# Kernel optimization log

Hardware: AMD Instinct MI355X
Metric: run time of the kernel (lower is better)

The kernel has to match this reference:

```python
import jax, jax.numpy as jnp
import numpy as np

N, D, M, H, FF, L = 8192, 14, 36, 256, 2048, 2  # rows, d_model, material feats, mlp hidden, ffn, layers
EPS = 1e-5


def _ln(x, g, b):
    mu = jnp.mean(x, axis=-1, keepdims=True)
    var = jnp.mean((x - mu) ** 2, axis=-1, keepdims=True)
    return (x - mu) * jax.lax.rsqrt(var + EPS) * g + b


def setup_inputs() -> dict:
    key = jax.random.key(0)
    ks = iter(jax.random.split(key, 32))
    p = lambda shape, fan: jax.random.normal(next(ks), shape, jnp.float32) * (fan ** -0.5)
    return {
        "x": jax.random.normal(next(ks), (N, D), jnp.float32),
        "y": jax.random.normal(next(ks), (N, M), jnp.float32),
        # 2 post-LN TransformerEncoderLayers (nhead=1, dim_feedforward=2048, relu)
        "attn_wqkv": p((L, 3 * D, D), D), "attn_bqkv": p((L, 3 * D), D),
        "attn_wo": p((L, D, D), D), "attn_bo": p((L, D), D),
        "ln1_g": jnp.ones((L, D)), "ln1_b": jnp.zeros((L, D)),
        "ff_w1": p((L, FF, D), D), "ff_b1": p((L, FF), D),
        "ff_w2": p((L, D, FF), FF), "ff_b2": p((L, D), FF),
        "ln2_g": jnp.ones((L, D)), "ln2_b": jnp.zeros((L, D)),
        "fc1_w": p((D, D), D), "fc1_b": p((D,), D),
        "fc2_w": p((1, D), D), "fc2_b": p((1,), D),
        "fc3_w": p((H, D + M + 1), D + M + 1), "fc3_b": p((H,), D + M + 1),
        "fc4_w": p((H, H), H), "fc4_b": p((H,), H),
        "fc5_w": p((1, H), H), "fc5_b": p((1,), H),
    }


def reference(x, y, attn_wqkv, attn_bqkv, attn_wo, attn_bo, ln1_g, ln1_b,
              ff_w1, ff_b1, ff_w2, ff_b2, ln2_g, ln2_b,
              fc1_w, fc1_b, fc2_w, fc2_b, fc3_w, fc3_b, fc4_w, fc4_b, fc5_w, fc5_b):
    h = x  # [N, D]; batch of size 1 squeezed away
    for l in range(L):
        qkv = h @ attn_wqkv[l].T + attn_bqkv[l]            # [N, 3D]
        q, k, v = jnp.split(qkv, 3, axis=-1)
        scores = (q @ k.T) * (D ** -0.5)                   # [N, N]
        a = jax.nn.softmax(scores, axis=-1) @ v            # [N, D]
        a = a @ attn_wo[l].T + attn_bo[l]
        h = _ln(h + a, ln1_g[l], ln1_b[l])
        f = jax.nn.relu(h @ ff_w1[l].T + ff_b1[l]) @ ff_w2[l].T + ff_b2[l]
        h = _ln(h + f, ln2_g[l], ln2_b[l])
    x1 = h @ fc1_w.T + fc1_b                               # [N, D]
    size_out = (x1 @ fc2_w.T + fc2_b)[:, 0]                # [N]

    # batched replacement of the per-row python loop
    size_int = size_out.astype(jnp.int32)                  # trunc toward zero, like .int()
    size_f = size_int.astype(jnp.float32)[:, None]         # [N, 1]
    reg_in = jnp.concatenate([size_f, x, y], axis=1)       # [N, 1+D+M]
    r = jax.nn.relu(reg_in @ fc3_w.T + fc3_b)
    r = jax.nn.relu(r @ fc4_w.T + fc4_b)
    reg_values = (r @ fc5_w.T + fc5_b)[:, 0]               # [N]
    reg_values = jnp.where(size_int != 0, reg_values, 0.0)
    return size_out, reg_values
```

## Files before the change

### kernel.cpp

```cpp
#include <hip/hip_runtime.h>
#include <math.h>

#define NN 8192
#define DD 14
#define DP 16
#define FF 2048
#define HID 256
#define LN_EPS 1e-5f
#define NCH 16
#define NFCH 8
#define QSCALE (1.4426950408889634f / 3.7416573867739413f)

typedef short bf16x8 __attribute__((ext_vector_type(8)));
typedef float f32x4 __attribute__((ext_vector_type(4)));

#define LOAD16(dst, srcp) { \
  const float4* _p = (const float4*)(srcp); \
  float4 _a = _p[0], _b = _p[1], _c = _p[2], _d = _p[3]; \
  dst[0]=_a.x; dst[1]=_a.y; dst[2]=_a.z; dst[3]=_a.w; \
  dst[4]=_b.x; dst[5]=_b.y; dst[6]=_b.z; dst[7]=_b.w; \
  dst[8]=_c.x; dst[9]=_c.y; dst[10]=_c.z; dst[11]=_c.w; \
  dst[12]=_d.x; dst[13]=_d.y; dst[14]=_d.z; dst[15]=_d.w; }

#define STORE16(dstp, src) { \
  float4* _p = (float4*)(dstp); \
  _p[0] = make_float4(src[0], src[1], src[2], src[3]); \
  _p[1] = make_float4(src[4], src[5], src[6], src[7]); \
  _p[2] = make_float4(src[8], src[9], src[10], src[11]); \
  _p[3] = make_float4(src[12], src[13], src[14], src[15]); }

static __device__ __forceinline__ float fast_exp2(float x) {
#if __has_builtin(__builtin_amdgcn_exp2f)
  return __builtin_amdgcn_exp2f(x);
#else
  return exp2f(x);
#endif
}

static __device__ __forceinline__ unsigned short bf_hi(float x) {
  return (unsigned short)(__float_as_uint(x) >> 16);
}
static __device__ __forceinline__ float bf_hi_f(float x) {
  return __uint_as_float(__float_as_uint(x) & 0xffff0000u);
}

static __device__ __forceinline__ void split8(const float* pv, bf16x8* ph, bf16x8* pl) {
  #pragma unroll
  for (int i = 0; i < 8; i++) {
    unsigned int u = __float_as_uint(pv[i]);
    (*ph)[i] = (short)(u >> 16);
    float rr = pv[i] - __uint_as_float(u & 0xffff0000u);
    (*pl)[i] = (short)(__float_as_uint(rr) >> 16);
  }
}

static __device__ __forceinline__ void qkv_compute_store(
    int r, const float* hr, const float* __restrict__ wqkv,
    const float* __restrict__ bqkv, unsigned int* __restrict__ Qpack,
    unsigned int* __restrict__ KB1, unsigned int* __restrict__ KB2,
    unsigned short* __restrict__ VhiT, unsigned short* __restrict__ VloT) {
  float q[14], k[14], v[14];
  #pragma unroll 6
  for (int c = 0; c < 42; c++) {
    const float* w = wqkv + c * 14;
    float s = bqkv[c];
    #pragma unroll
    for (int d = 0; d < 14; d++) s = fmaf(hr[d], w[d], s);
    if (c < 14)       q[c] = s * QSCALE;
    else if (c < 28)  k[c - 14] = s;
    else              v[c - 28] = s;
  }
  unsigned int qp[16], k1[16], k2[16];
  unsigned short qh[14], ql[14], kh[14], kl[14];
  #pragma unroll
  for (int d = 0; d < 14; d++) {
    qh[d] = bf_hi(q[d]);
    ql[d] = bf_hi(q[d] - bf_hi_f(q[d]));
    kh[d] = bf_hi(k[d]);
    kl[d] = bf_hi(k[d] - bf_hi_f(k[d]));
  }
  #pragma unroll
  for (int i = 0; i < 7; i++) {
    qp[i]     = (unsigned int)qh[2*i] | ((unsigned int)qh[2*i+1] << 16);
    qp[8 + i] = (unsigned int)ql[2*i] | ((unsigned int)ql[2*i+1] << 16);
    k1[i]     = (unsigned int)kh[2*i] | ((unsigned int)kh[2*i+1] << 16);
    k1[8 + i] = k1[i];
    k2[i]     = (unsigned int)kl[2*i] | ((unsigned int)kl[2*i+1] << 16);
    k2[8 + i] = k2[i];
  }
  qp[7] = 0; qp[15] = 0; k1[7] = 0; k1[15] = 0; k2[7] = 0; k2[15] = 0;
  uint4* Qp4 = (uint4*)(Qpack + (size_t)r * 16);
  uint4* K14 = (uint4*)(KB1 + (size_t)r * 16);
  uint4* K24 = (uint4*)(KB2 + (size_t)r * 16);
  #pragma unroll
  for (int i = 0; i < 4; i++) {
    Qp4[i] = make_uint4(qp[4*i], qp[4*i+1], qp[4*i+2], qp[4*i+3]);
    K14[i] = make_uint4(k1[4*i], k1[4*i+1], k1[4*i+2], k1[4*i+3]);
    K24[i] = make_uint4(k2[4*i], k2[4*i+1], k2[4*i+2], k2[4*i+3]);
  }
  #pragma unroll
  for (int d = 0; d < 14; d++) {
    VhiT[(size_t)d * NN + r] = bf_hi(v[d]);
    VloT[(size_t)d * NN + r] = bf_hi(v[d] - bf_hi_f(v[d]));
  }
  VhiT[(size_t)14 * NN + r] = 0x3F80;
  VhiT[(size_t)15 * NN + r] = 0;
  VloT[(size_t)14 * NN + r] = 0;
  VloT[(size_t)15 * NN + r] = 0;
}

static __device__ __forceinline__ void store_apack(unsigned int* dst, const float* o) {
  unsigned int qp[16];
  unsigned short hh[14], ll[14];
  #pragma unroll
  for (int d = 0; d < 14; d++) {
    hh[d] = bf_hi(o[d]);
    ll[d] = bf_hi(o[d] - bf_hi_f(o[d]));
  }
  #pragma unroll
  for (int i = 0; i < 7; i++) {
    qp[i]     = (unsigned int)hh[2*i] | ((unsigned int)hh[2*i+1] << 16);
    qp[8 + i] = (unsigned int)ll[2*i] | ((unsigned int)ll[2*i+1] << 16);
  }
  qp[7] = 0; qp[15] = 0;
  uint4* d4 = (uint4*)dst;
  #pragma unroll
  for (int i = 0; i < 4; i++)
    d4[i] = make_uint4(qp[4*i], qp[4*i+1], qp[4*i+2], qp[4*i+3]);
}

__global__ void pack_all(const float* __restrict__ w3, const float* __restrict__ w4,
                         const float* __restrict__ ffw1, const float* __restrict__ ffw2,
                         const float* __restrict__ x, const float* __restrict__ wqkv,
                         const float* __restrict__ bqkv, float* __restrict__ h,
                         unsigned int* __restrict__ Qpack,
                         unsigned int* __restrict__ KB1, unsigned int* __restrict__ KB2,
                         unsigned short* __restrict__ VhiT, unsigned short* __restrict__ VloT,
                         unsigned short* __restrict__ B3h, unsigned short* __restrict__ B3l,
                         unsigned short* __restrict__ B4h, unsigned short* __restrict__ B4l,
                         unsigned int* __restrict__ W1B1, unsigned int* __restrict__ W1B2,
                         unsigned short* __restrict__ W2h, unsigned short* __restrict__ W2l) {
  const int blk = blockIdx.x, tid = threadIdx.x;
  if (blk < 32) {
    int t = blk * 256 + tid;
    int lane = t & 63, ks = (t >> 6) & 7, nt = t >> 9;
    int n = nt * 16 + (lane & 15);
    int k0 = ks * 32 + (lane >> 4) * 8;
    unsigned int h4[4], l4[4];
    #pragma unroll
    for (int jj = 0; jj < 4; jj++) {
      unsigned short h2[2], l2[2];
      #pragma unroll
      for (int e = 0; e < 2; e++) {
        float v = w4[(size_t)n * 256 + k0 + jj * 2 + e];
        h2[e] = bf_hi(v);
        l2[e] = bf_hi(v - bf_hi_f(v));
      }
      h4[jj] = (unsigned int)h2[0] | ((unsigned int)h2[1] << 16);
      l4[jj] = (unsigned int)l2[0] | ((unsigned int)l2[1] << 16);
    }
    ((uint4*)B4h)[t] = make_uint4(h4[0], h4[1], h4[2], h4[3]);
    ((uint4*)B4l)[t] = make_uint4(l4[0], l4[1], l4[2], l4[3]);
    if (ks < 2) {
      int fi = (nt * 2 + ks) * 64 + lane;
      #pragma unroll
      for (int jj = 0; jj < 4; jj++) {
        unsigned short h2[2], l2[2];
        #pragma unroll
        for (int e = 0; e < 2; e++) {
          int k = k0 + jj * 2 + e;
          float v = (k < 51) ? w3[(size_t)n * 51 + k] : 0.f;
          h2[e] = bf_hi(v);
          l2[e] = bf_hi(v - bf_hi_f(v));
        }
        h4[jj] = (unsigned int)h2[0] | ((unsigned int)h2[1] << 16);
        l4[jj] = (unsigned int)l2[0] | ((unsigned int)l2[1] << 16);
      }
      ((uint4*)B3h)[fi] = make_uint4(h4[0], h4[1], h4[2], h4[3]);
      ((uint4*)B3l)[fi] = make_uint4(l4[0], l4[1], l4[2], l4[3]);
    }
  } else if (blk < 48) {
    int t = (blk - 32) * 256 + tid;
    int l = t >> 11, j = t & 2047;
    const float* wrow = ffw1 + ((size_t)l * FF + j) * 14;
    unsigned int k1[16], k2[16];
    unsigned short kh[14], kl[14];
    #pragma unroll
    for (int d = 0; d < 14; d++) {
      float v = wrow[d];
      kh[d] = bf_hi(v);
      kl[d] = bf_hi(v - bf_hi_f(v));
    }
    #pragma unroll
    for (int i = 0; i < 7; i++) {
      k1[i] = (unsigned int)kh[2*i] | ((unsigned int)kh[2*i+1] << 16);
      k1[8 + i] = k1[i];
      k2[i] = (unsigned int)kl[2*i] | ((unsigned int)kl[2*i+1] << 16);
      k2[8 + i] = k2[i];
    }
    k1[7] = 0; k1[15] = 0; k2[7] = 0; k2[15] = 0;
    uint4* d1 = (uint4*)(W1B1 + (size_t)t * 16);
    uint4* d2 = (uint4*)(W1B2 + (size_t)t * 16);
    #pragma unroll
    for (int i = 0; i < 4; i++) {
      d1[i] = make_uint4(k1[4*i], k1[4*i+1], k1[4*i+2], k1[4*i+3]);
      d2[i] = make_uint4(k2[4*i], k2[4*i+1], k2[4*i+2], k2[4*i+3]);
    }
  } else if (blk < 64) {
    int t = (blk - 48) * 256 + tid;
    int l = t >> 11, j = t & 2047;
    #pragma unroll
    for (int d = 0; d < 16; d++) {
      float v = (d < 14) ? ffw2[((size_t)l * 14 + d) * FF + j] : 0.f;
      W2h[((size_t)l * 16 + d) * FF + j] = bf_hi(v);
      W2l[((size_t)l * 16 + d) * FF + j] = bf_hi(v - bf_hi_f(v));
    }
  } else {
    int r = (blk - 64) * 256 + tid;
    float hr[16];
    #pragma unroll
    for (int d = 0; d < 14; d++) hr[d] = x[(size_t)r * 14 + d];
    hr[14] = 0.f; hr[15] = 0.f;
    STORE16(h + (size_t)r * DP, hr);
    qkv_compute_store(r, hr, wqkv, bqkv, Qpack, KB1, KB2, VhiT, VloT);
  }
}

__global__ __launch_bounds__(256, 4) void attn_mfma(
    const unsigned int* __restrict__ Qpack, const unsigned int* __restrict__ KB1,
    const unsigned int* __restrict__ KB2, const unsigned short* __restrict__ VhiT,
    const unsigned short* __restrict__ VloT, float* __restrict__ part) {
  __shared__ float Plds[4][32][36];
  const int tid = threadIdx.x;
  const int wave = tid >> 6;
  const int lane = tid & 63;
  const int lo4 = lane & 15;
  const int hi4 = lane >> 4;
  const int qbase = blockIdx.x * 128 + wave * 32;
  const int kbase0 = blockIdx.y * 512;

  const bf16x8* Qp = (const bf16x8*)Qpack;
  const bf16x8* B1 = (const bf16x8*)KB1;
  const bf16x8* B2 = (const bf16x8*)KB2;
  const bf16x8* Vh = (const bf16x8*)VhiT;
  const bf16x8* Vl = (const bf16x8*)VloT;

  bf16x8 aQ0 = Qp[(size_t)(qbase + lo4) * 4 + hi4];
  bf16x8 aQ1 = Qp[(size_t)(qbase + 16 + lo4) * 4 + hi4];
  f32x4 acc0 = {0.f, 0.f, 0.f, 0.f};
  f32x4 acc1 = {0.f, 0.f, 0.f, 0.f};
  const f32x4 zero = {0.f, 0.f, 0.f, 0.f};

  for (int c = 0; c < 16; c++) {
    const int kb = kbase0 + c * 32;
    bf16x8 b1g0 = B1[(size_t)(kb + lo4) * 4 + hi4];
    bf16x8 b2g0 = B2[(size_t)(kb + lo4) * 4 + hi4];
    bf16x8 b1g1 = B1[(size_t)(kb + 16 + lo4) * 4 + hi4];
    bf16x8 b2g1 = B2[(size_t)(kb + 16 + lo4) * 4 + hi4];
    bf16x8 vh = Vh[(size_t)lo4 * 1024 + (kb >> 3) + hi4];
    bf16x8 vl = Vl[(size_t)lo4 * 1024 + (kb >> 3) + hi4];

    f32x4 s00 = __builtin_amdgcn_mfma_f32_16x16x32_bf16(aQ0, b1g0, zero, 0, 0, 0);
    f32x4 s01 = __builtin_amdgcn_mfma_f32_16x16x32_bf16(aQ0, b1g1, zero, 0, 0, 0);
    f32x4 s10 = __builtin_amdgcn_mfma_f32_16x16x32_bf16(aQ1, b1g0, zero, 0, 0, 0);
    f32x4 s11 = __builtin_amdgcn_mfma_f32_16x16x32_bf16(aQ1, b1g1, zero, 0, 0, 0);
    s00 = __builtin_amdgcn_mfma_f32_16x16x32_bf16(aQ0, b2g0, s00, 0, 0, 0);
    s01 = __builtin_amdgcn_mfma_f32_16x16x32_bf16(aQ0, b2g1, s01, 0, 0, 0);
    s10 = __builtin_amdgcn_mfma_f32_16x16x32_bf16(aQ1, b2g0, s10, 0, 0, 0);
    s11 = __builtin_amdgcn_mfma_f32_16x16x32_bf16(aQ1, b2g1, s11, 0, 0, 0);
    #pragma unroll
    for (int reg = 0; reg < 4; reg++) {
      Plds[wave][hi4 * 4 + reg][lo4]           = fast_exp2(s00[reg]);
      Plds[wave][hi4 * 4 + reg][16 + lo4]      = fast_exp2(s01[reg]);
      Plds[wave][16 + hi4 * 4 + reg][lo4]      = fast_exp2(s10[reg]);
      Plds[wave][16 + hi4 * 4 + reg][16 + lo4] = fast_exp2(s11[reg]);
    }
    __asm__ volatile("s_waitcnt lgkmcnt(0)" ::: "memory");
    const float4* p0 = (const float4*)&Plds[wave][lo4][hi4 * 8];
    const float4* p1 = (const float4*)&Plds[wave][16 + lo4][hi4 * 8];
    float4 a0 = p0[0], a1 = p0[1], c0 = p1[0], c1 = p1[1];
    float pv0[8] = {a0.x, a0.y, a0.z, a0.w, a1.x, a1.y, a1.z, a1.w};
    float pv1[8] = {c0.x, c0.y, c0.z, c0.w, c1.x, c1.y, c1.z, c1.w};
    bf16x8 ph0, pl0, ph1, pl1;
    split8(pv0, &ph0, &pl0);
    split8(pv1, &ph1, &pl1);
    acc0 = __builtin_amdgcn_mfma_f32_16x16x32_bf16(ph0, vh, acc0, 0, 0, 0);
    acc1 = __builtin_amdgcn_mfma_f32_16x16x32_bf16(ph1, vh, acc1, 0, 0, 0);
    acc0 = __builtin_amdgcn_mfma_f32_16x16x32_bf16(pl0, vh, acc0, 0, 0, 0);
    acc1 = __builtin_amdgcn_mfma_f32_16x16x32_bf16(pl1, vh, acc1, 0, 0, 0);
    acc0 = __builtin_amdgcn_mfma_f32_16x16x32_bf16(ph0, vl, acc0, 0, 0, 0);
    acc1 = __builtin_amdgcn_mfma_f32_16x16x32_bf16(ph1, vl, acc1, 0, 0, 0);
    __asm__ volatile("s_waitcnt lgkmcnt(0)" ::: "memory");
  }
  float* pbase = part + (size_t)blockIdx.y * NN * 16;
  #pragma unroll
  for (int reg = 0; reg < 4; reg++) {
    int row0 = qbase + hi4 * 4 + reg;
    pbase[(size_t)row0 * 16 + lo4] = acc0[reg];
    pbase[(size_t)(row0 + 16) * 16 + lo4] = acc1[reg];
  }
}

__global__ void attn_comb_ln1(float* __restrict__ h, const float* __restrict__ part,
                              const float* __restrict__ wo, const float* __restrict__ bo,
                              const float* __restrict__ g, const float* __restrict__ b,
                              unsigned int* __restrict__ Hpack) {
  int t = blockIdx.x * 128 + threadIdx.x;
  int r = t >> 2, q = t & 3;
  float L = 0.f;
  float A[14];
  #pragma unroll
  for (int d = 0; d < 14; d++) A[d] = 0.f;
  #pragma unroll
  for (int c = q; c < NCH; c += 4) {
    float p[16];
    LOAD16(p, part + ((size_t)c * NN + r) * 16);
    L += p[14];
    #pragma unroll
    for (int d = 0; d < 14; d++) A[d] += p[d];
  }
  #pragma unroll
  for (int off = 1; off < 4; off <<= 1) {
    L += __shfl_xor(L, off, 64);
    #pragma unroll
    for (int d = 0; d < 14; d++) A[d] += __shfl_xor(A[d], off, 64);
  }
  if (q == 0) {
    float inv = 1.f / L;
    float a[14];
    #pragma unroll
    for (int d = 0; d < 14; d++) a[d] = A[d] * inv;
    float hr[16];
    LOAD16(hr, h + (size_t)r * DP);
    float xx[14];
    #pragma unroll
    for (int i = 0; i < 14; i++) {
      float s = bo[i];
      #pragma unroll
      for (int d = 0; d < 14; d++) s = fmaf(wo[i * 14 + d], a[d], s);
      xx[i] = hr[i] + s;
    }
    float mu = 0.f;
    #pragma unroll
    for (int i = 0; i < 14; i++) mu += xx[i];
    mu *= (1.f / 14.f);
    float var = 0.f;
    #pragma unroll
    for (int i = 0; i < 14; i++) { float tt = xx[i] - mu; var = fmaf(tt, tt, var); }
    var *= (1.f / 14.f);
    float rs = rsqrtf(var + LN_EPS);
    float o[16];
    #pragma unroll
    for (int i = 0; i < 14; i++) o[i] = fmaf((xx[i] - mu) * rs, g[i], b[i]);
    o[14] = 0.f; o[15] = 0.f;
    STORE16(h + (size_t)r * DP, o);
    store_apack(Hpack + (size_t)r * 16, o);
  }
}

__global__ __launch_bounds__(256, 4) void ffn_mfma(
    const unsigned int* __restrict__ Hpack, const unsigned int* __restrict__ W1B1,
    const unsigned int* __restrict__ W1B2, const unsigned short* __restrict__ W2h,
    const unsigned short* __restrict__ W2l, const float* __restrict__ b1,
    float* __restrict__ part) {
  __shared__ float Plds[4][32][36];
  const int tid = threadIdx.x;
  const int wave = tid >> 6;
  const int lane = tid & 63;
  const int lo4 = lane & 15;
  const int hi4 = lane >> 4;
  const int qbase = blockIdx.x * 128 + wave * 32;
  const int jbase0 = blockIdx.y * 256;

  const bf16x8* Hp = (const bf16x8*)Hpack;
  const bf16x8* B1 = (const bf16x8*)W1B1;
  const bf16x8* B2 = (const bf16x8*)W1B2;
  const bf16x8* Vh = (const bf16x8*)W2h;
  const bf16x8* Vl = (const bf16x8*)W2l;

  bf16x8 aH0 = Hp[(size_t)(qbase + lo4) * 4 + hi4];
  bf16x8 aH1 = Hp[(size_t)(qbase + 16 + lo4) * 4 + hi4];
  f32x4 acc0 = {0.f, 0.f, 0.f, 0.f};
  f32x4 acc1 = {0.f, 0.f, 0.f, 0.f};
  const f32x4 zero = {0.f, 0.f, 0.f, 0.f};

  for (int c = 0; c < 8; c++) {
    const int jb = jbase0 + c * 32;
    bf16x8 b1g0 = B1[(size_t)(jb + lo4) * 4 + hi4];
    bf16x8 b2g0 = B2[(size_t)(jb + lo4) * 4 + hi4];
    bf16x8 b1g1 = B1[(size_t)(jb + 16 + lo4) * 4 + hi4];
    bf16x8 b2g1 = B2[(size_t)(jb + 16 + lo4) * 4 + hi4];
    bf16x8 vh = Vh[(size_t)lo4 * 256 + (jb >> 3) + hi4];
    bf16x8 vl = Vl[(size_t)lo4 * 256 + (jb >> 3) + hi4];
    float bb0 = b1[jb + lo4];
    float bb1 = b1[jb + 16 + lo4];

    f32x4 s00 = __builtin_amdgcn_mfma_f32_16x16x32_bf16(aH0, b1g0, zero, 0, 0, 0);
    f32x4 s01 = __builtin_amdgcn_mfma_f32_16x16x32_bf16(aH0, b1g1, zero, 0, 0, 0);
    f32x4 s10 = __builtin_amdgcn_mfma_f32_16x16x32_bf16(aH1, b1g0, zero, 0, 0, 0);
    f32x4 s11 = __builtin_amdgcn_mfma_f32_16x16x32_bf16(aH1, b1g1, zero, 0, 0, 0);
    s00 = __builtin_amdgcn_mfma_f32_16x16x32_bf16(aH0, b2g0, s00, 0, 0, 0);
    s01 = __builtin_amdgcn_mfma_f32_16x16x32_bf16(aH0, b2g1, s01, 0, 0, 0);
    s10 = __builtin_amdgcn_mfma_f32_16x16x32_bf16(aH1, b2g0, s10, 0, 0, 0);
    s11 = __builtin_amdgcn_mfma_f32_16x16x32_bf16(aH1, b2g1, s11, 0, 0, 0);
    #pragma unroll
    for (int reg = 0; reg < 4; reg++) {
      Plds[wave][hi4 * 4 + reg][lo4]           = fmaxf(s00[reg] + bb0, 0.f);
      Plds[wave][hi4 * 4 + reg][16 + lo4]      = fmaxf(s01[reg] + bb1, 0.f);
      Plds[wave][16 + hi4 * 4 + reg][lo4]      = fmaxf(s10[reg] + bb0, 0.f);
      Plds[wave][16 + hi4 * 4 + reg][16 + lo4] = fmaxf(s11[reg] + bb1, 0.f);
    }
    __asm__ volatile("s_waitcnt lgkmcnt(0)" ::: "memory");
    const float4* p0 = (const float4*)&Plds[wave][lo4][hi4 * 8];
    const float4* p1 = (const float4*)&Plds[wave][16 + lo4][hi4 * 8];
    float4 a0 = p0[0], a1 = p0[1], c0 = p1[0], c1 = p1[1];
    float pv0[8] = {a0.x, a0.y, a0.z, a0.w, a1.x, a1.y, a1.z, a1.w};
    float pv1[8] = {c0.x, c0.y, c0.z, c0.w, c1.x, c1.y, c1.z, c1.w};
    bf16x8 th0, tl0, th1, tl1;
    split8(pv0, &th0, &tl0);
    split8(pv1, &th1, &tl1);
    acc0 = __builtin_amdgcn_mfma_f32_16x16x32_bf16(th0, vh, acc0, 0, 0, 0);
    acc1 = __builtin_amdgcn_mfma_f32_16x16x32_bf16(th1, vh, acc1, 0, 0, 0);
    acc0 = __builtin_amdgcn_mfma_f32_16x16x32_bf16(tl0, vh, acc0, 0, 0, 0);
    acc1 = __builtin_amdgcn_mfma_f32_16x16x32_bf16(tl1, vh, acc1, 0, 0, 0);
    acc0 = __builtin_amdgcn_mfma_f32_16x16x32_bf16(th0, vl, acc0, 0, 0, 0);
    acc1 = __builtin_amdgcn_mfma_f32_16x16x32_bf16(th1, vl, acc1, 0, 0, 0);
    __asm__ volatile("s_waitcnt lgkmcnt(0)" ::: "memory");
  }
  float* pbase = part + (size_t)blockIdx.y * NN * 16;
  #pragma unroll
  for (int reg = 0; reg < 4; reg++) {
    int row0 = qbase + hi4 * 4 + reg;
    pbase[(size_t)row0 * 16 + lo4] = acc0[reg];
    pbase[(size_t)(row0 + 16) * 16 + lo4] = acc1[reg];
  }
}

__global__ void ffn_ln2_qkv(float* __restrict__ h, const float* __restrict__ part,
                            const float* __restrict__ b2, const float* __restrict__ g,
                            const float* __restrict__ b,
                            const float* __restrict__ wqkv, const float* __restrict__ bqkv,
                            unsigned int* __restrict__ Qpack,
                            unsigned int* __restrict__ KB1, unsigned int* __restrict__ KB2,
                            unsigned short* __restrict__ VhiT,
                            unsigned short* __restrict__ VloT) {
  int t = blockIdx.x * 128 + threadIdx.x;
  int r = t >> 2, q = t & 3;
  float f[14];
  #pragma unroll
  for (int d = 0; d < 14; d++) f[d] = 0.f;
  #pragma unroll
  for (int c = q; c < NFCH; c += 4) {
    float p[16];
    LOAD16(p, part + ((size_t)c * NN + r) * 16);
    #pragma unroll
    for (int d = 0; d < 14; d++) f[d] += p[d];
  }
  #pragma unroll
  for (int off = 1; off < 4; off <<= 1) {
    #pragma unroll
    for (int d = 0; d < 14; d++) f[d] += __shfl_xor(f[d], off, 64);
  }
  if (q == 0) {
    float hr[16];
    LOAD16(hr, h + (size_t)r * DP);
    float xx[14];
    #pragma unroll
    for (int i = 0; i < 14; i++) xx[i] = hr[i] + f[i] + b2[i];
    float mu = 0.f;
    #pragma unroll
    for (int i = 0; i < 14; i++) mu += xx[i];
    mu *= (1.f / 14.f);
    float var = 0.f;
    #pragma unroll
    for (int i = 0; i < 14; i++) { float tt = xx[i] - mu; var = fmaf(tt, tt, var); }
    var *= (1.f / 14.f);
    float rs = rsqrtf(var + LN_EPS);
    float o[16];
    #pragma unroll
    for (int i = 0; i < 14; i++) o[i] = fmaf((xx[i] - mu) * rs, g[i], b[i]);
    o[14] = 0.f; o[15] = 0.f;
    STORE16(h + (size_t)r * DP, o);
    qkv_compute_store(r, o, wqkv, bqkv, Qpack, KB1, KB2, VhiT, VloT);
  }
}

__global__ __launch_bounds__(256, 4) void tail_fused(
    const float* __restrict__ h, const float* __restrict__ part,
    const float* __restrict__ b2, const float* __restrict__ g, const float* __restrict__ b,
    const float* __restrict__ fc1w, const float* __restrict__ fc1b,
    const float* __restrict__ fc2w, const float* __restrict__ fc2b,
    const float* __restrict__ x, const float* __restrict__ y,
    const unsigned short* __restrict__ B3h, const unsigned short* __restrict__ B3l,
    const float* __restrict__ b3,
    const unsigned short* __restrict__ B4h, const unsigned short* __restrict__ B4l,
    const float* __restrict__ b4,
    const float* __restrict__ w5, const float* __restrict__ b5,
    float* __restrict__ out, float* __restrict__ outr) {
  __shared__ alignas(16) unsigned short Ah[16][72], Al[16][72];
  __shared__ alignas(16) unsigned short R1h[16][264], R1l[16][264];
  __shared__ float sred[4][16][16];
  __shared__ float szf[16];
  const int tid = threadIdx.x;
  const int wave = tid >> 6;
  const int lane = tid & 63;
  const int lo4 = lane & 15;
  const int hi4 = lane >> 4;
  const int rbase = blockIdx.x * 16;

  if (tid < 128) {
    int m = tid >> 3, c = tid & 7;
    int r = rbase + m;
    float p[16];
    LOAD16(p, part + ((size_t)c * NN + r) * 16);
    float f[14];
    #pragma unroll
    for (int d = 0; d < 14; d++) f[d] = p[d];
    #pragma unroll
    for (int off = 1; off < 8; off <<= 1) {
      #pragma unroll
      for (int d = 0; d < 14; d++) f[d] += __shfl_xor(f[d], off, 64);
    }
    if (c == 0) {
      float hr[16];
      LOAD16(hr, h + (size_t)r * DP);
      float xx[14];
      #pragma unroll
      for (int i = 0; i < 14; i++) xx[i] = hr[i] + f[i] + b2[i];
      float mu = 0.f;
      #pragma unroll
      for (int i = 0; i < 14; i++) mu += xx[i];
      mu *= (1.f / 14.f);
      float var = 0.f;
      #pragma unroll
      for (int i = 0; i < 14; i++) { float tt = xx[i] - mu; var = fmaf(tt, tt, var); }
      var *= (1.f / 14.f);
      float rs = rsqrtf(var + LN_EPS);
      float o[14];
      #pragma unroll
      for (int i = 0; i < 14; i++) o[i] = fmaf((xx[i] - mu) * rs, g[i], b[i]);
      float s = fc2b[0];
      #pragma unroll
      for (int i = 0; i < 14; i++) {
        float tt = fc1b[i];
        #pragma unroll
        for (int d = 0; d < 14; d++) tt = fmaf(fc1w[i * 14 + d], o[d], tt);
        s = fmaf(tt, fc2w[i], s);
      }
      out[r] = s;
      int si = (int)s;
      szf[m] = (float)si;
    }
  }
  __syncthreads();

  for (int idx = tid; idx < 16 * 64; idx += 256) {
    int m = idx >> 6, k = idx & 63;
    int r = rbase + m;
    float v = 0.f;
    if (k == 0)       v = szf[m];
    else if (k < 15)  v = x[(size_t)r * 14 + (k - 1)];
    else if (k < 51)  v = y[(size_t)r * 36 + (k - 15)];
    Ah[m][k] = bf_hi(v);
    Al[m][k] = bf_hi(v - bf_hi_f(v));
  }
  __syncthreads();

  const f32x4 zero = {0.f, 0.f, 0.f, 0.f};
  f32x4 acc[4];
  #pragma unroll
  for (int nt = 0; nt < 4; nt++) acc[nt] = zero;

  #pragma unroll
  for (int ks = 0; ks < 2; ks++) {
    bf16x8 ah = *(const bf16x8*)&Ah[lo4][ks * 32 + hi4 * 8];
    bf16x8 al = *(const bf16x8*)&Al[lo4][ks * 32 + hi4 * 8];
    #pragma unroll
    for (int nt = 0; nt < 4; nt++) {
      int fi = ((wave * 4 + nt) * 2 + ks) * 64 + lane;
      bf16x8 bh = ((const bf16x8*)B3h)[fi];
      bf16x8 bl = ((const bf16x8*)B3l)[fi];
      acc[nt] = __builtin_amdgcn_mfma_f32_16x16x32_bf16(ah, bh, acc[nt], 0, 0, 0);
      acc[nt] = __builtin_amdgcn_mfma_f32_16x16x32_bf16(al, bh, acc[nt], 0, 0, 0);
      acc[nt] = __builtin_amdgcn_mfma_f32_16x16x32_bf16(ah, bl, acc[nt], 0, 0, 0);
    }
  }
  #pragma unroll
  for (int nt = 0; nt < 4; nt++) {
    int n = (wave * 4 + nt) * 16 + lo4;
    float bb = b3[n];
    #pragma unroll
    for (int reg = 0; reg < 4; reg++) {
      int m = hi4 * 4 + reg;
      float v = fmaxf(acc[nt][reg] + bb, 0.f);
      R1h[m][n] = bf_hi(v);
      R1l[m][n] = bf_hi(v - bf_hi_f(v));
    }
  }
  __syncthreads();

  #pragma unroll
  for (int nt = 0; nt < 4; nt++) acc[nt] = zero;
  #pragma unroll
  for (int ks = 0; ks < 8; ks++) {
    bf16x8 ah = *(const bf16x8*)&R1h[lo4][ks * 32 + hi4 * 8];
    bf16x8 al = *(const bf16x8*)&R1l[lo4][ks * 32 + hi4 * 8];
    #pragma unroll
    for (int nt = 0; nt < 4; nt++) {
      int fi = ((wave * 4 + nt) * 8 + ks) * 64 + lane;
      bf16x8 bh = ((const bf16x8*)B4h)[fi];
      bf16x8 bl = ((const bf16x8*)B4l)[fi];
      acc[nt] = __builtin_amdgcn_mfma_f32_16x16x32_bf16(ah, bh, acc[nt], 0, 0, 0);
      acc[nt] = __builtin_amdgcn_mfma_f32_16x16x32_bf16(al, bh, acc[nt], 0, 0, 0);
      acc[nt] = __builtin_amdgcn_mfma_f32_16x16x32_bf16(ah, bl, acc[nt], 0, 0, 0);
    }
  }
  float s[4] = {0.f, 0.f, 0.f, 0.f};
  #pragma unroll
  for (int nt = 0; nt < 4; nt++) {
    int n = (wave * 4 + nt) * 16 + lo4;
    float bb = b4[n], ww = w5[n];
    #pragma unroll
    for (int reg = 0; reg < 4; reg++)
      s[reg] = fmaf(fmaxf(acc[nt][reg] + bb, 0.f), ww, s[reg]);
  }
  #pragma unroll
  for (int reg = 0; reg < 4; reg++) sred[wave][hi4 * 4 + reg][lo4] = s[reg];
  __syncthreads();

  if (tid < 16) {
    float t = b5[0];
    #pragma unroll
    for (int w = 0; w < 4; w++) {
      const float4* p = (const float4*)&sred[w][tid][0];
      float4 a0 = p[0], a1 = p[1], a2 = p[2], a3 = p[3];
      t += ((a0.x + a0.y) + (a0.z + a0.w)) + ((a1.x + a1.y) + (a1.z + a1.w)) +
           ((a2.x + a2.y) + (a2.z + a2.w)) + ((a3.x + a3.y) + (a3.z + a3.w));
    }
    float sz = szf[tid];
    outr[rbase + tid] = (sz != 0.f) ? t : 0.f;
  }
}

extern "C" void kernel_launch(void* const* d_in, const int* in_sizes, int n_in,
                              void* d_out, int out_size, void* d_ws, size_t ws_size,
                              hipStream_t stream) {
  const float* x    = (const float*)d_in[0];
  const float* y    = (const float*)d_in[1];
  const float* wqkv = (const float*)d_in[2];
  const float* bqkv = (const float*)d_in[3];
  const float* wo   = (const float*)d_in[4];
  const float* bo   = (const float*)d_in[5];
  const float* ln1g = (const float*)d_in[6];
  const float* ln1b = (const float*)d_in[7];
  const float* ffw1 = (const float*)d_in[8];
  const float* ffb1 = (const float*)d_in[9];
  const float* ffw2 = (const float*)d_in[10];
  const float* ffb2 = (const float*)d_in[11];
  const float* ln2g = (const float*)d_in[12];
  const float* ln2b = (const float*)d_in[13];
  const float* fc1w = (const float*)d_in[14];
  const float* fc1b = (const float*)d_in[15];
  const float* fc2w = (const float*)d_in[16];
  const float* fc2b = (const float*)d_in[17];
  const float* fc3w = (const float*)d_in[18];
  const float* fc3b = (const float*)d_in[19];
  const float* fc4w = (const float*)d_in[20];
  const float* fc4b = (const float*)d_in[21];
  const float* fc5w = (const float*)d_in[22];
  const float* fc5b = (const float*)d_in[23];

  float* ws = (float*)d_ws;
  float*          h     = ws;
  unsigned int*   Qpack = (unsigned int*)(ws + 131072);
  unsigned int*   KB1   = (unsigned int*)(ws + 262144);
  unsigned int*   KB2   = (unsigned int*)(ws + 393216);
  unsigned short* VhiT  = (unsigned short*)(ws + 524288);
  unsigned short* VloT  = (unsigned short*)(ws + 589824);
  unsigned int*   Hpack = (unsigned int*)(ws + 655360);
  float*          part  = ws + 786432;
  unsigned short* B3h   = (unsigned short*)(ws + 2891776);
  unsigned short* B3l   = (unsigned short*)(ws + 2899968);
  unsigned short* B4h   = (unsigned short*)(ws + 2908160);
  unsigned short* B4l   = (unsigned short*)(ws + 2940928);
  unsigned int*   W1B1  = (unsigned int*)(ws + 2973696);
  unsigned int*   W1B2  = (unsigned int*)(ws + 3039232);
  unsigned short* W2h   = (unsigned short*)(ws + 3104768);
  unsigned short* W2l   = (unsigned short*)(ws + 3137536);

  float* out = (float*)d_out;

  pack_all<<<96, 256, 0, stream>>>(fc3w, fc4w, ffw1, ffw2, x, wqkv, bqkv, h,
                                   Qpack, KB1, KB2, VhiT, VloT,
                                   B3h, B3l, B4h, B4l, W1B1, W1B2, W2h, W2l);
  for (int l = 0; l < 2; l++) {
    attn_mfma<<<dim3(64, NCH), 256, 0, stream>>>(Qpack, KB1, KB2, VhiT, VloT, part);
    attn_comb_ln1<<<256, 128, 0, stream>>>(h, part, wo + (size_t)l * 196,
                                           bo + (size_t)l * 14, ln1g + (size_t)l * 14,
                                           ln1b + (size_t)l * 14, Hpack);
    ffn_mfma<<<dim3(64, NFCH), 256, 0, stream>>>(
        Hpack, W1B1 + (size_t)l * 2048 * 16, W1B2 + (size_t)l * 2048 * 16,
        W2h + (size_t)l * 16 * FF, W2l + (size_t)l * 16 * FF,
        ffb1 + (size_t)l * FF, part);
    if (l == 0) {
      ffn_ln2_qkv<<<256, 128, 0, stream>>>(h, part, ffb2, ln2g, ln2b,
                                           wqkv + 42 * 14, bqkv + 42,
                                           Qpack, KB1, KB2, VhiT, VloT);
    }
  }
  tail_fused<<<512, 256, 0, stream>>>(h, part, ffb2 + 14, ln2g + 14, ln2b + 14,
                                      fc1w, fc1b, fc2w, fc2b, x, y,
                                      B3h, B3l, fc3b, B4h, B4l, fc4b,
                                      fc5w, fc5b, out, out + NN);
}
```

Measured before the change: 258.5 us.

## Fuse split-K partial reductions into attention and FFN kernels via in-block LDS reduction

The attention and FFN MFMA kernels no longer split the key/hidden dimension across grid blocks and write partials to global memory. Each block now owns 32 query rows, and its 8 waves split the key/FF range among themselves. Partials are reduced in shared memory and the following LayerNorm/QKV/tail epilogue runs in the same kernel. This drops the separate combine kernels, the global partial buffer traffic and several launches. In exchange there are fewer, larger blocks (256 blocks of 512 threads), longer per-wave loops, and the epilogue is serialized onto 32 threads per block.

```diff
diff --git a/kernel.cpp b/kernel.cpp
--- a/kernel.cpp
+++ b/kernel.cpp
@@ -7,8 +7,6 @@
 #define FF 2048
 #define HID 256
 #define LN_EPS 1e-5f
-#define NCH 16
-#define NFCH 8
 #define QSCALE (1.4426950408889634f / 3.7416573867739413f)
 
 typedef short bf16x8 __attribute__((ext_vector_type(8)));
@@ -226,18 +224,21 @@
   }
 }
 
-__global__ __launch_bounds__(256, 4) void attn_mfma(
+__global__ __launch_bounds__(512, 2) void attn_flash(
     const unsigned int* __restrict__ Qpack, const unsigned int* __restrict__ KB1,
     const unsigned int* __restrict__ KB2, const unsigned short* __restrict__ VhiT,
-    const unsigned short* __restrict__ VloT, float* __restrict__ part) {
-  __shared__ float Plds[4][32][36];
+    const unsigned short* __restrict__ VloT, float* __restrict__ h,
+    const float* __restrict__ wo, const float* __restrict__ bo,
+    const float* __restrict__ g, const float* __restrict__ b,
+    unsigned int* __restrict__ Hpack) {
+  __shared__ float Plds[8][32][36];
+  __shared__ float sacc[8][32][16];
   const int tid = threadIdx.x;
   const int wave = tid >> 6;
   const int lane = tid & 63;
   const int lo4 = lane & 15;
   const int hi4 = lane >> 4;
-  const int qbase = blockIdx.x * 128 + wave * 32;
-  const int kbase0 = blockIdx.y * 512;
+  const int qbase = blockIdx.x * 32;
 
   const bf16x8* Qp = (const bf16x8*)Qpack;
   const bf16x8* B1 = (const bf16x8*)KB1;
@@ -251,8 +252,9 @@
   f32x4 acc1 = {0.f, 0.f, 0.f, 0.f};
   const f32x4 zero = {0.f, 0.f, 0.f, 0.f};
 
-  for (int c = 0; c < 16; c++) {
-    const int kb = kbase0 + c * 32;
+  const int kstart = wave * 1024;
+  for (int c = 0; c < 32; c++) {
+    const int kb = kstart + c * 32;
     bf16x8 b1g0 = B1[(size_t)(kb + lo4) * 4 + hi4];
     bf16x8 b2g0 = B2[(size_t)(kb + lo4) * 4 + hi4];
     bf16x8 b1g1 = B1[(size_t)(kb + 16 + lo4) * 4 + hi4];
@@ -292,44 +294,29 @@
     acc1 = __builtin_amdgcn_mfma_f32_16x16x32_bf16(ph1, vl, acc1, 0, 0, 0);
     __asm__ volatile("s_waitcnt lgkmcnt(0)" ::: "memory");
   }
-  float* pbase = part + (size_t)blockIdx.y * NN * 16;
+
   #pragma unroll
   for (int reg = 0; reg < 4; reg++) {
-    int row0 = qbase + hi4 * 4 + reg;
-    pbase[(size_t)row0 * 16 + lo4] = acc0[reg];
-    pbase[(size_t)(row0 + 16) * 16 + lo4] = acc1[reg];
-  }
-}
-
-__global__ void attn_comb_ln1(float* __restrict__ h, const float* __restrict__ part,
-                              const float* __restrict__ wo, const float* __restrict__ bo,
-                              const float* __restrict__ g, const float* __restrict__ b,
-                              unsigned int* __restrict__ Hpack) {
-  int t = blockIdx.x * 128 + threadIdx.x;
-  int r = t >> 2, q = t & 3;
-  float L = 0.f;
-  float A[14];
-  #pragma unroll
-  for (int d = 0; d < 14; d++) A[d] = 0.f;
-  #pragma unroll
-  for (int c = q; c < NCH; c += 4) {
-    float p[16];
-    LOAD16(p, part + ((size_t)c * NN + r) * 16);
-    L += p[14];
-    #pragma unroll
-    for (int d = 0; d < 14; d++) A[d] += p[d];
-  }
-  #pragma unroll
-  for (int off = 1; off < 4; off <<= 1) {
-    L += __shfl_xor(L, off, 64);
-    #pragma unroll
-    for (int d = 0; d < 14; d++) A[d] += __shfl_xor(A[d], off, 64);
-  }
-  if (q == 0) {
+    sacc[wave][hi4 * 4 + reg][lo4] = acc0[reg];
+    sacc[wave][16 + hi4 * 4 + reg][lo4] = acc1[reg];
+  }
+  __syncthreads();
+  {
+    int qq = tid >> 4, col = tid & 15;
+    float v = 0.f;
+    #pragma unroll
+    for (int w = 0; w < 8; w++) v += sacc[w][qq][col];
+    sacc[0][qq][col] = v;
+  }
+  __syncthreads();
+
+  if (tid < 32) {
+    int r = qbase + tid;
+    float L = sacc[0][tid][14];
     float inv = 1.f / L;
     float a[14];
     #pragma unroll
-    for (int d = 0; d < 14; d++) a[d] = A[d] * inv;
+    for (int d = 0; d < 14; d++) a[d] = sacc[0][tid][d] * inv;
     float hr[16];
     LOAD16(hr, h + (size_t)r * DP);
     float xx[14];
@@ -358,19 +345,24 @@
   }
 }
 
-__global__ __launch_bounds__(256, 4) void ffn_mfma(
-    const unsigned int* __restrict__ Hpack, const unsigned int* __restrict__ W1B1,
-    const unsigned int* __restrict__ W1B2, const unsigned short* __restrict__ W2h,
-    const unsigned short* __restrict__ W2l, const float* __restrict__ b1,
-    float* __restrict__ part) {
-  __shared__ float Plds[4][32][36];
+__global__ __launch_bounds__(512, 2) void ffn_flash_qkv(
+    float* __restrict__ h, const unsigned int* __restrict__ Hpack,
+    const unsigned int* __restrict__ W1B1, const unsigned int* __restrict__ W1B2,
+    const unsigned short* __restrict__ W2h, const unsigned short* __restrict__ W2l,
+    const float* __restrict__ b1, const float* __restrict__ b2,
+    const float* __restrict__ g, const float* __restrict__ bb,
+    const float* __restrict__ wqkv, const float* __restrict__ bqkv,
+    unsigned int* __restrict__ Qpack, unsigned int* __restrict__ KB1,
+    unsigned int* __restrict__ KB2, unsigned short* __restrict__ VhiT,
+    unsigned short* __restrict__ VloT) {
+  __shared__ float Plds[8][32][36];
+  __shared__ float sacc[8][32][16];
   const int tid = threadIdx.x;
   const int wave = tid >> 6;
   const int lane = tid & 63;
   const int lo4 = lane & 15;
   const int hi4 = lane >> 4;
-  const int qbase = blockIdx.x * 128 + wave * 32;
-  const int jbase0 = blockIdx.y * 256;
+  const int qbase = blockIdx.x * 32;
 
   const bf16x8* Hp = (const bf16x8*)Hpack;
   const bf16x8* B1 = (const bf16x8*)W1B1;
@@ -384,8 +376,9 @@
   f32x4 acc1 = {0.f, 0.f, 0.f, 0.f};
   const f32x4 zero = {0.f, 0.f, 0.f, 0.f};
 
+  const int jstart = wave * 256;
   for (int c = 0; c < 8; c++) {
-    const int jb = jbase0 + c * 32;
+    const int jb = jstart + c * 32;
     bf16x8 b1g0 = B1[(size_t)(jb + lo4) * 4 + hi4];
     bf16x8 b2g0 = B2[(size_t)(jb + lo4) * 4 + hi4];
     bf16x8 b1g1 = B1[(size_t)(jb + 16 + lo4) * 4 + hi4];
@@ -427,46 +420,29 @@
     acc1 = __builtin_amdgcn_mfma_f32_16x16x32_bf16(th1, vl, acc1, 0, 0, 0);
     __asm__ volatile("s_waitcnt lgkmcnt(0)" ::: "memory");
   }
-  float* pbase = part + (size_t)blockIdx.y * NN * 16;
+
   #pragma unroll
   for (int reg = 0; reg < 4; reg++) {
-    int row0 = qbase + hi4 * 4 + reg;
-    pbase[(size_t)row0 * 16 + lo4] = acc0[reg];
-    pbase[(size_t)(row0 + 16) * 16 + lo4] = acc1[reg];
-  }
-}
-
-__global__ void ffn_ln2_qkv(float* __restrict__ h, const float* __restrict__ part,
-                            const float* __restrict__ b2, const float* __restrict__ g,
-                            const float* __restrict__ b,
-                            const float* __restrict__ wqkv, const float* __restrict__ bqkv,
-                            unsigned int* __restrict__ Qpack,
-                            unsigned int* __restrict__ KB1, unsigned int* __restrict__ KB2,
-                            unsigned short* __restrict__ VhiT,
-                            unsigned short* __restrict__ VloT) {
-  int t = blockIdx.x * 128 + threadIdx.x;
-  int r = t >> 2, q = t & 3;
-  float f[14];
-  #pragma unroll
-  for (int d = 0; d < 14; d++) f[d] = 0.f;
-  #pragma unroll
-  for (int c = q; c < NFCH; c += 4) {
-    float p[16];
-    LOAD16(p, part + ((size_t)c * NN + r) * 16);
-    #pragma unroll
-    for (int d = 0; d < 14; d++) f[d] += p[d];
-  }
-  #pragma unroll
-  for (int off = 1; off < 4; off <<= 1) {
-    #pragma unroll
-    for (int d = 0; d < 14; d++) f[d] += __shfl_xor(f[d], off, 64);
-  }
-  if (q == 0) {
+    sacc[wave][hi4 * 4 + reg][lo4] = acc0[reg];
+    sacc[wave][16 + hi4 * 4 + reg][lo4] = acc1[reg];
+  }
+  __syncthreads();
+  {
+    int qq = tid >> 4, col = tid & 15;
+    float v = 0.f;
+    #pragma unroll
+    for (int w = 0; w < 8; w++) v += sacc[w][qq][col];
+    sacc[0][qq][col] = v;
+  }
+  __syncthreads();
+
+  if (tid < 32) {
+    int r = qbase + tid;
     float hr[16];
     LOAD16(hr, h + (size_t)r * DP);
     float xx[14];
     #pragma unroll
-    for (int i = 0; i < 14; i++) xx[i] = hr[i] + f[i] + b2[i];
+    for (int i = 0; i < 14; i++) xx[i] = hr[i] + sacc[0][tid][i] + b2[i];
     float mu = 0.f;
     #pragma unroll
     for (int i = 0; i < 14; i++) mu += xx[i];
@@ -478,15 +454,18 @@
     float rs = rsqrtf(var + LN_EPS);
     float o[16];
     #pragma unroll
-    for (int i = 0; i < 14; i++) o[i] = fmaf((xx[i] - mu) * rs, g[i], b[i]);
+    for (int i = 0; i < 14; i++) o[i] = fmaf((xx[i] - mu) * rs, g[i], bb[i]);
     o[14] = 0.f; o[15] = 0.f;
     STORE16(h + (size_t)r * DP, o);
     qkv_compute_store(r, o, wqkv, bqkv, Qpack, KB1, KB2, VhiT, VloT);
   }
 }
 
-__global__ __launch_bounds__(256, 4) void tail_fused(
-    const float* __restrict__ h, const float* __restrict__ part,
+__global__ __launch_bounds__(256, 4) void ffn_tail(
+    const float* __restrict__ h, const unsigned int* __restrict__ Hpack,
+    const unsigned int* __restrict__ W1B1, const unsigned int* __restrict__ W1B2,
+    const unsigned short* __restrict__ W2h, const unsigned short* __restrict__ W2l,
+    const float* __restrict__ b1,
     const float* __restrict__ b2, const float* __restrict__ g, const float* __restrict__ b,
     const float* __restrict__ fc1w, const float* __restrict__ fc1b,
     const float* __restrict__ fc2w, const float* __restrict__ fc2b,
@@ -497,6 +476,8 @@
     const float* __restrict__ b4,
     const float* __restrict__ w5, const float* __restrict__ b5,
     float* __restrict__ out, float* __restrict__ outr) {
+  __shared__ float PldsT[4][16][36];
+  __shared__ float saccT[4][16][16];
   __shared__ alignas(16) unsigned short Ah[16][72], Al[16][72];
   __shared__ alignas(16) unsigned short R1h[16][264], R1l[16][264];
   __shared__ float sred[4][16][16];
@@ -507,50 +488,90 @@
   const int lo4 = lane & 15;
   const int hi4 = lane >> 4;
   const int rbase = blockIdx.x * 16;
-
-  if (tid < 128) {
-    int m = tid >> 3, c = tid & 7;
-    int r = rbase + m;
-    float p[16];
-    LOAD16(p, part + ((size_t)c * NN + r) * 16);
-    float f[14];
-    #pragma unroll
-    for (int d = 0; d < 14; d++) f[d] = p[d];
-    #pragma unroll
-    for (int off = 1; off < 8; off <<= 1) {
+  const f32x4 zero = {0.f, 0.f, 0.f, 0.f};
+
+  {
+    const bf16x8* Hp = (const bf16x8*)Hpack;
+    const bf16x8* B1 = (const bf16x8*)W1B1;
+    const bf16x8* B2 = (const bf16x8*)W1B2;
+    const bf16x8* Vh = (const bf16x8*)W2h;
+    const bf16x8* Vl = (const bf16x8*)W2l;
+    bf16x8 aH0 = Hp[(size_t)(rbase + lo4) * 4 + hi4];
+    f32x4 acc0 = zero;
+    const int jstart = wave * 512;
+    for (int c = 0; c < 16; c++) {
+      const int jb = jstart + c * 32;
+      bf16x8 b1g0 = B1[(size_t)(jb + lo4) * 4 + hi4];
+      bf16x8 b2g0 = B2[(size_t)(jb + lo4) * 4 + hi4];
+      bf16x8 b1g1 = B1[(size_t)(jb + 16 + lo4) * 4 + hi4];
+      bf16x8 b2g1 = B2[(size_t)(jb + 16 + lo4) * 4 + hi4];
+      bf16x8 vh = Vh[(size_t)lo4 * 256 + (jb >> 3) + hi4];
+      bf16x8 vl = Vl[(size_t)lo4 * 256 + (jb >> 3) + hi4];
+      float bb0 = b1[jb + lo4];
+      float bb1 = b1[jb + 16 + lo4];
+
+      f32x4 s00 = __builtin_amdgcn_mfma_f32_16x16x32_bf16(aH0, b1g0, zero, 0, 0, 0);
+      f32x4 s01 = __builtin_amdgcn_mfma_f32_16x16x32_bf16(aH0, b1g1, zero, 0, 0, 0);
+      s00 = __builtin_amdgcn_mfma_f32_16x16x32_bf16(aH0, b2g0, s00, 0, 0, 0);
+      s01 = __builtin_amdgcn_mfma_f32_16x16x32_bf16(aH0, b2g1, s01, 0, 0, 0);
       #pragma unroll
-      for (int d = 0; d < 14; d++) f[d] += __shfl_xor(f[d], off, 64);
-    }
-    if (c == 0) {
-      float hr[16];
-      LOAD16(hr, h + (size_t)r * DP);
-      float xx[14];
+      for (int reg = 0; reg < 4; reg++) {
+        PldsT[wave][hi4 * 4 + reg][lo4]      = fmaxf(s00[reg] + bb0, 0.f);
+        PldsT[wave][hi4 * 4 + reg][16 + lo4] = fmaxf(s01[reg] + bb1, 0.f);
+      }
+      __asm__ volatile("s_waitcnt lgkmcnt(0)" ::: "memory");
+      const float4* p0 = (const float4*)&PldsT[wave][lo4][hi4 * 8];
+      float4 a0 = p0[0], a1 = p0[1];
+      float pv0[8] = {a0.x, a0.y, a0.z, a0.w, a1.x, a1.y, a1.z, a1.w};
+      bf16x8 th0, tl0;
+      split8(pv0, &th0, &tl0);
+      acc0 = __builtin_amdgcn_mfma_f32_16x16x32_bf16(th0, vh, acc0, 0, 0, 0);
+      acc0 = __builtin_amdgcn_mfma_f32_16x16x32_bf16(tl0, vh, acc0, 0, 0, 0);
+      acc0 = __builtin_amdgcn_mfma_f32_16x16x32_bf16(th0, vl, acc0, 0, 0, 0);
+      __asm__ volatile("s_waitcnt lgkmcnt(0)" ::: "memory");
+    }
+    #pragma unroll
+    for (int reg = 0; reg < 4; reg++)
+      saccT[wave][hi4 * 4 + reg][lo4] = acc0[reg];
+  }
+  __syncthreads();
+  {
+    int qq = tid >> 4, col = tid & 15;
+    float v = saccT[0][qq][col] + saccT[1][qq][col] + saccT[2][qq][col] + saccT[3][qq][col];
+    saccT[0][qq][col] = v;
+  }
+  __syncthreads();
+
+  if (tid < 16) {
+    int r = rbase + tid;
+    float hr[16];
+    LOAD16(hr, h + (size_t)r * DP);
+    float xx[14];
+    #pragma unroll
+    for (int i = 0; i < 14; i++) xx[i] = hr[i] + saccT[0][tid][i] + b2[i];
+    float mu = 0.f;
+    #pragma unroll
+    for (int i = 0; i < 14; i++) mu += xx[i];
+    mu *= (1.f / 14.f);
+    float var = 0.f;
+    #pragma unroll
+    for (int i = 0; i < 14; i++) { float tt = xx[i] - mu; var = fmaf(tt, tt, var); }
+    var *= (1.f / 14.f);
+    float rs = rsqrtf(var + LN_EPS);
+    float o[14];
+    #pragma unroll
+    for (int i = 0; i < 14; i++) o[i] = fmaf((xx[i] - mu) * rs, g[i], b[i]);
+    float s = fc2b[0];
+    #pragma unroll
+    for (int i = 0; i < 14; i++) {
+      float tt = fc1b[i];
       #pragma unroll
-      for (int i = 0; i < 14; i++) xx[i] = hr[i] + f[i] + b2[i];
-      float mu = 0.f;
-      #pragma unroll
-      for (int i = 0; i < 14; i++) mu += xx[i];
-      mu *= (1.f / 14.f);
-      float var = 0.f;
-      #pragma unroll
-      for (int i = 0; i < 14; i++) { float tt = xx[i] - mu; var = fmaf(tt, tt, var); }
-      var *= (1.f / 14.f);
-      float rs = rsqrtf(var + LN_EPS);
-      float o[14];
-      #pragma unroll
-      for (int i = 0; i < 14; i++) o[i] = fmaf((xx[i] - mu) * rs, g[i], b[i]);
-      float s = fc2b[0];
-      #pragma unroll
-      for (int i = 0; i < 14; i++) {
-        float tt = fc1b[i];
-        #pragma unroll
-        for (int d = 0; d < 14; d++) tt = fmaf(fc1w[i * 14 + d], o[d], tt);
-        s = fmaf(tt, fc2w[i], s);
-      }
-      out[r] = s;
-      int si = (int)s;
-      szf[m] = (float)si;
-    }
+      for (int d = 0; d < 14; d++) tt = fmaf(fc1w[i * 14 + d], o[d], tt);
+      s = fmaf(tt, fc2w[i], s);
+    }
+    out[r] = s;
+    int si = (int)s;
+    szf[tid] = (float)si;
   }
   __syncthreads();
 
@@ -566,11 +587,9 @@
   }
   __syncthreads();
 
-  const f32x4 zero = {0.f, 0.f, 0.f, 0.f};
   f32x4 acc[4];
   #pragma unroll
   for (int nt = 0; nt < 4; nt++) acc[nt] = zero;
-
   #pragma unroll
   for (int ks = 0; ks < 2; ks++) {
     bf16x8 ah = *(const bf16x8*)&Ah[lo4][ks * 32 + hi4 * 8];
@@ -588,11 +607,11 @@
   #pragma unroll
   for (int nt = 0; nt < 4; nt++) {
     int n = (wave * 4 + nt) * 16 + lo4;
-    float bb = b3[n];
+    float bbv = b3[n];
     #pragma unroll
     for (int reg = 0; reg < 4; reg++) {
       int m = hi4 * 4 + reg;
-      float v = fmaxf(acc[nt][reg] + bb, 0.f);
+      float v = fmaxf(acc[nt][reg] + bbv, 0.f);
       R1h[m][n] = bf_hi(v);
       R1l[m][n] = bf_hi(v - bf_hi_f(v));
     }
@@ -615,17 +634,17 @@
       acc[nt] = __builtin_amdgcn_mfma_f32_16x16x32_bf16(ah, bl, acc[nt], 0, 0, 0);
     }
   }
-  float s[4] = {0.f, 0.f, 0.f, 0.f};
+  float s4[4] = {0.f, 0.f, 0.f, 0.f};
   #pragma unroll
   for (int nt = 0; nt < 4; nt++) {
     int n = (wave * 4 + nt) * 16 + lo4;
-    float bb = b4[n], ww = w5[n];
+    float bbv = b4[n], ww = w5[n];
     #pragma unroll
     for (int reg = 0; reg < 4; reg++)
-      s[reg] = fmaf(fmaxf(acc[nt][reg] + bb, 0.f), ww, s[reg]);
-  }
-  #pragma unroll
-  for (int reg = 0; reg < 4; reg++) sred[wave][hi4 * 4 + reg][lo4] = s[reg];
+      s4[reg] = fmaf(fmaxf(acc[nt][reg] + bbv, 0.f), ww, s4[reg]);
+  }
+  #pragma unroll
+  for (int reg = 0; reg < 4; reg++) sred[wave][hi4 * 4 + reg][lo4] = s4[reg];
   __syncthreads();
 
   if (tid < 16) {
@@ -678,7 +697,6 @@
   unsigned short* VhiT  = (unsigned short*)(ws + 524288);
   unsigned short* VloT  = (unsigned short*)(ws + 589824);
   unsigned int*   Hpack = (unsigned int*)(ws + 655360);
-  float*          part  = ws + 786432;
   unsigned short* B3h   = (unsigned short*)(ws + 2891776);
   unsigned short* B3l   = (unsigned short*)(ws + 2899968);
   unsigned short* B4h   = (unsigned short*)(ws + 2908160);
@@ -693,23 +711,20 @@
   pack_all<<<96, 256, 0, stream>>>(fc3w, fc4w, ffw1, ffw2, x, wqkv, bqkv, h,
                                    Qpack, KB1, KB2, VhiT, VloT,
                                    B3h, B3l, B4h, B4l, W1B1, W1B2, W2h, W2l);
-  for (int l = 0; l < 2; l++) {
-    attn_mfma<<<dim3(64, NCH), 256, 0, stream>>>(Qpack, KB1, KB2, VhiT, VloT, part);
-    attn_comb_ln1<<<256, 128, 0, stream>>>(h, part, wo + (size_t)l * 196,
-                                           bo + (size_t)l * 14, ln1g + (size_t)l * 14,
-                                           ln1b + (size_t)l * 14, Hpack);
-    ffn_mfma<<<dim3(64, NFCH), 256, 0, stream>>>(
-        Hpack, W1B1 + (size_t)l * 2048 * 16, W1B2 + (size_t)l * 2048 * 16,
-        W2h + (size_t)l * 16 * FF, W2l + (size_t)l * 16 * FF,
-        ffb1 + (size_t)l * FF, part);
-    if (l == 0) {
-      ffn_ln2_qkv<<<256, 128, 0, stream>>>(h, part, ffb2, ln2g, ln2b,
-                                           wqkv + 42 * 14, bqkv + 42,
-                                           Qpack, KB1, KB2, VhiT, VloT);
-    }
-  }
-  tail_fused<<<512, 256, 0, stream>>>(h, part, ffb2 + 14, ln2g + 14, ln2b + 14,
-                                      fc1w, fc1b, fc2w, fc2b, x, y,
-                                      B3h, B3l, fc3b, B4h, B4l, fc4b,
-                                      fc5w, fc5b, out, out + NN);
-}
+
+  attn_flash<<<256, 512, 0, stream>>>(Qpack, KB1, KB2, VhiT, VloT, h,
+                                      wo, bo, ln1g, ln1b, Hpack);
+  ffn_flash_qkv<<<256, 512, 0, stream>>>(h, Hpack, W1B1, W1B2, W2h, W2l,
+                                         ffb1, ffb2, ln2g, ln2b,
+                                         wqkv + 42 * 14, bqkv + 42,
+                                         Qpack, KB1, KB2, VhiT, VloT);
+  attn_flash<<<256, 512, 0, stream>>>(Qpack, KB1, KB2, VhiT, VloT, h,
+                                      wo + 196, bo + 14, ln1g + 14, ln1b + 14, Hpack);
+  ffn_tail<<<512, 256, 0, stream>>>(h, Hpack,
+                                    W1B1 + (size_t)2048 * 16, W1B2 + (size_t)2048 * 16,
+                                    W2h + (size_t)16 * FF, W2l + (size_t)16 * FF,
+                                    ffb1 + FF, ffb2 + 14, ln2g + 14, ln2b + 14,
+                                    fc1w, fc1b, fc2w, fc2b, x, y,
+                                    B3h, B3l, fc3b, B4h, B4l, fc4b,
+                                    fc5w, fc5b, out, out + NN);
+}
```

After: 244.9 us. -5.2%, faster.
